# Kernel tuning notes

Measured on AMD Instinct MI355X. Metric: run time of the kernel, lower is better.

## Reference

```python
import jax, jax.numpy as jnp
import numpy as np

B, S, D, H = 4, 2048, 1024, 16
DK = D // H


def setup_inputs() -> dict:
    key = jax.random.key(0)
    kx, kq, kk, kv, ko = jax.random.split(key, 5)
    scale = D ** -0.5
    return {
        "x": jax.random.normal(kx, (B, S, D), dtype=jnp.float32),
        "W_q": jax.random.normal(kq, (D, D), dtype=jnp.float32) * scale,
        "W_k": jax.random.normal(kk, (D, D), dtype=jnp.float32) * scale,
        "W_v": jax.random.normal(kv, (D, D), dtype=jnp.float32) * scale,
        "W_o": jax.random.normal(ko, (D, D), dtype=jnp.float32) * scale,
    }


def reference(x, W_q, W_k, W_v, W_o):
    b, s, d = x.shape
    # projections: x @ W.T  (weights stored [out, in])
    def proj(W):
        return (x @ W.T).reshape(b, s, H, DK).transpose(0, 2, 1, 3)  # [b,h,s,dk]
    Q, K, V = proj(W_q), proj(W_k), proj(W_v)
    scores = jnp.einsum('bhqd,bhkd->bhqk', Q, K) * (DK ** -0.5)
    causal = jnp.tril(jnp.ones((s, s), dtype=bool))
    scores = jnp.where(causal, scores, -jnp.inf)
    attn = jax.nn.softmax(scores, axis=-1)
    out = jnp.einsum('bhqk,bhkd->bhqd', attn, V)  # [b,h,s,dk]
    out = out.transpose(0, 2, 1, 3).reshape(b, s, d)
    return out @ W_o.T
```

## Files before the change

kernel.cpp:

```cpp
#include <hip/hip_runtime.h>
#include <stdint.h>

#define B_ 4
#define S_ 2048
#define D_ 1024
#define H_ 16
#define DK_ 64
#define M_ (B_*S_)

typedef __attribute__((ext_vector_type(8))) short bhalf8;
typedef __attribute__((ext_vector_type(4))) short bhalf4;
typedef __attribute__((ext_vector_type(4))) float floatx4;
typedef unsigned short bfu;
typedef unsigned int u32;

__device__ __forceinline__ bfu f2bf(float f) {
  union { float f; u32 u; } v; v.f = f;
  u32 r = v.u + 0x7FFFu + ((v.u >> 16) & 1u);
  return (bfu)(r >> 16);
}

__device__ __forceinline__ u32 cvtpk(float a, float b) {
  u32 r;
  asm("v_cvt_pk_bf16_f32 %0, %1, %2" : "=v"(r) : "v"(a), "v"(b));
  return r;
}

__device__ __forceinline__ void gll16(const bfu* g, bfu* l) {
  __builtin_amdgcn_global_load_lds((__attribute__((address_space(1))) void*)g,
                                   (__attribute__((address_space(3))) void*)l,
                                   16, 0, 0);
}

__global__ void cvt_f32_bf16(const float* __restrict__ src, bfu* __restrict__ dst, int n) {
  int i = (blockIdx.x * blockDim.x + threadIdx.x) * 4;
  if (i >= n) return;
  float4 v = *(const float4*)(src + i);
  ushort4 o;
  o.x = f2bf(v.x); o.y = f2bf(v.y); o.z = f2bf(v.z); o.w = f2bf(v.w);
  *(ushort4*)(dst + i) = o;
}

__device__ __forceinline__ void gemm_core_gll(const bfu* __restrict__ A,
                                              const bfu* __restrict__ Bw,
                                              bfu* aT, bfu* bT,
                                              int m0, int bn0,
                                              floatx4 (&acc)[4][4])
{
  const int tid  = threadIdx.x;
  const int lane = tid & 63;
  const int g    = lane >> 4;
  const int i16  = lane & 15;
  const int w    = tid >> 6;
  const int wm   = w >> 1, wn = w & 1;

  const int lrow = lane >> 3;
  const int scol = ((lane & 7) ^ lrow) << 3;
  const bfu* As = A  + (size_t)(m0  + w * 32 + lrow) * D_ + scol;
  const bfu* Bs = Bw + (size_t)(bn0 + w * 32 + lrow) * D_ + scol;

  for (int k0 = 0; k0 < D_; k0 += 64) {
#pragma unroll
    for (int j = 0; j < 4; ++j) {
      gll16(As + (size_t)j * 8 * D_ + k0, aT + (w * 4 + j) * 512);
      gll16(Bs + (size_t)j * 8 * D_ + k0, bT + (w * 4 + j) * 512);
    }
    __syncthreads();
    const char* aTc = (const char*)aT;
    const char* bTc = (const char*)bT;
#pragma unroll
    for (int kb = 0; kb < 2; ++kb) {
      bhalf8 af[4], bf[4];
#pragma unroll
      for (int f = 0; f < 4; ++f) {
        int arow = wm * 64 + f * 16 + i16;
        af[f] = *(const bhalf8*)(aTc + arow * 128 + ((kb * 64 + g * 16) ^ ((arow & 7) << 4)));
        int brow = wn * 64 + f * 16 + i16;
        bf[f] = *(const bhalf8*)(bTc + brow * 128 + ((kb * 64 + g * 16) ^ ((brow & 7) << 4)));
      }
#pragma unroll
      for (int fm = 0; fm < 4; ++fm)
#pragma unroll
        for (int fn = 0; fn < 4; ++fn)
          acc[fm][fn] = __builtin_amdgcn_mfma_f32_16x16x32_bf16(af[fm], bf[fn], acc[fm][fn], 0, 0, 0);
    }
    __syncthreads();
  }
}

__global__ __launch_bounds__(256) void qkv_gemm(const bfu* __restrict__ xb,
                                                const bfu* __restrict__ wqkv,
                                                bfu* __restrict__ Qd,
                                                bfu* __restrict__ Kd,
                                                bfu* __restrict__ Vtd)
{
  __shared__ bfu aT[8192], bT[8192];
  const int bid = blockIdx.x;
  const int wi   = bid >> 3;
  const int xblk = wi >> 3;
  const int y    = ((bid & 7) << 3) | (wi & 7);
  const int m0   = y * 128;
  const int z    = xblk >> 3;
  const int n0   = (xblk & 7) * 128;
  const int bn0  = xblk * 128;

  floatx4 acc[4][4] = {};
  gemm_core_gll(xb, wqkv, aT, bT, m0, bn0, acc);

  bfu* dst = (z == 0) ? Qd : (z == 1) ? Kd : Vtd;
  const int lane = threadIdx.x & 63;
  const int g = lane >> 4, i16 = lane & 15;
  const int w = threadIdx.x >> 6, wm = w >> 1, wn = w & 1;
#pragma unroll
  for (int fm = 0; fm < 4; ++fm) {
#pragma unroll
    for (int fn = 0; fn < 4; ++fn) {
      int col = n0 + wn * 64 + fn * 16 + i16;
      int h = col >> 6, dk = col & 63;
#pragma unroll
      for (int r = 0; r < 4; ++r) {
        int mrow = m0 + wm * 64 + fm * 16 + g * 4 + r;
        int b = mrow >> 11, s = mrow & (S_ - 1);
        size_t idx = (z == 2)
            ? ((size_t)((b * H_ + h) * DK_ + dk)) * S_ + s
            : ((size_t)((b * H_ + h) * S_ + s)) * DK_ + dk;
        dst[idx] = f2bf(acc[fm][fn][r]);
      }
    }
  }
}

__global__ __launch_bounds__(256) void out_gemm(const bfu* __restrict__ Ab,
                                                const bfu* __restrict__ wob,
                                                float* __restrict__ out)
{
  __shared__ bfu aT[8192], bT[8192];
  const int bid = blockIdx.x;
  const int wi   = bid >> 3;
  const int xblk = wi >> 3;
  const int y    = ((bid & 7) << 3) | (wi & 7);
  const int m0   = y * 128;
  const int n0   = xblk * 128;

  floatx4 acc[4][4] = {};
  gemm_core_gll(Ab, wob, aT, bT, m0, n0, acc);

  const int lane = threadIdx.x & 63;
  const int g = lane >> 4, i16 = lane & 15;
  const int w = threadIdx.x >> 6, wm = w >> 1, wn = w & 1;
#pragma unroll
  for (int fm = 0; fm < 4; ++fm)
#pragma unroll
    for (int fn = 0; fn < 4; ++fn) {
      int col = n0 + wn * 64 + fn * 16 + i16;
#pragma unroll
      for (int r = 0; r < 4; ++r) {
        int mrow = m0 + wm * 64 + fm * 16 + g * 4 + r;
        out[(size_t)mrow * D_ + col] = acc[fm][fn][r];
      }
    }
}

template<int BUF>
__device__ __forceinline__ void attn_tile(const char* smem, int t, int ntw, int qr,
                                          int koff0, int koff1, const int (&voff)[4],
                                          bhalf8 qa0, bhalf8 qa1, int g, int i16,
                                          floatx4 (&ot)[4], float& mC2, float& lp)
{
  const float C2 = 0.125f * 1.44269504f;
  floatx4 sa[4] = {};
#pragma unroll
  for (int cb = 0; cb < 4; ++cb) {
    bhalf8 kf0 = *(const bhalf8*)(smem + BUF + cb * 2048 + koff0);
    bhalf8 kf1 = *(const bhalf8*)(smem + BUF + cb * 2048 + koff1);
    sa[cb] = __builtin_amdgcn_mfma_f32_16x16x32_bf16(kf0, qa0, sa[cb], 0, 0, 0);
    sa[cb] = __builtin_amdgcn_mfma_f32_16x16x32_bf16(kf1, qa1, sa[cb], 0, 0, 0);
  }
  if (t == ntw - 1) {
    const int kv0 = t * 64;
#pragma unroll
    for (int cb = 0; cb < 4; ++cb)
#pragma unroll
      for (int r = 0; r < 4; ++r)
        if (kv0 + cb * 16 + g * 4 + r > qr + i16) sa[cb][r] = -3.0e38f;
  }
  float pm = sa[0][0];
#pragma unroll
  for (int cb = 0; cb < 4; ++cb)
#pragma unroll
    for (int r = 0; r < 4; ++r)
      pm = fmaxf(pm, sa[cb][r]);
  pm = fmaxf(pm, __shfl_xor(pm, 16));
  pm = fmaxf(pm, __shfl_xor(pm, 32));
  const float pmC2 = pm * C2;
  if (!__all(pmC2 - mC2 <= 8.0f)) {
    const float nmax = fmaxf(mC2, pmC2);
    const float al = exp2f(mC2 - nmax);
    mC2 = nmax;
    lp *= al;
#pragma unroll
    for (int da = 0; da < 4; ++da)
#pragma unroll
      for (int r = 0; r < 4; ++r)
        ot[da][r] *= al;
  }
  const float nm = -mC2;
  u32 pk[8];
  float ps = 0.f;
#pragma unroll
  for (int cb = 0; cb < 4; ++cb) {
    float p0 = exp2f(__builtin_fmaf(sa[cb][0], C2, nm));
    float p1 = exp2f(__builtin_fmaf(sa[cb][1], C2, nm));
    float p2 = exp2f(__builtin_fmaf(sa[cb][2], C2, nm));
    float p3 = exp2f(__builtin_fmaf(sa[cb][3], C2, nm));
    ps += (p0 + p1) + (p2 + p3);
    pk[cb * 2]     = cvtpk(p0, p1);
    pk[cb * 2 + 1] = cvtpk(p2, p3);
  }
  lp += ps;
#pragma unroll
  for (int da = 0; da < 4; ++da) {
#pragma unroll
    for (int cb = 0; cb < 4; ++cb) {
      bhalf4 vf = *(const bhalf4*)(smem + BUF + voff[cb] + da * 2048);
      union { u32 u[2]; bhalf4 h; } pu;
      pu.u[0] = pk[cb * 2]; pu.u[1] = pk[cb * 2 + 1];
      ot[da] = __builtin_amdgcn_mfma_f32_16x16x16bf16_1k(vf, pu.h, ot[da], 0, 0, 0);
    }
  }
}

__global__ __launch_bounds__(512, 4) void attn_kernel(const bfu* __restrict__ Q,
                                                      const bfu* __restrict__ Kc,
                                                      const bfu* __restrict__ Vt,
                                                      bfu* __restrict__ Oc)
{
  __shared__ char smem[2 * 16384];
  const int tid = threadIdx.x;
  const int lane = tid & 63;
  const int w = tid >> 6;
  const int g = lane >> 4, i16 = lane & 15;
  const int sw = (i16 & 7) << 4;
  const int bh = blockIdx.x;
  const int y  = blockIdx.y;
  const int spine = 2 * y + 2;
  const int ntw = 2 * y + 1 + (w >> 2);
  const int qr = y * 128 + w * 16;

  const bfu* Qb = Q  + (size_t)bh * S_ * DK_;
  const bfu* Kb = Kc + (size_t)bh * S_ * DK_;
  const bfu* Vb = Vt + (size_t)bh * DK_ * S_;
  const int b = bh >> 4, h = bh & 15;

  const int srow = tid >> 3;
  const int scolb = (tid & 7) * 16;
  const bfu* kgp = Kb + srow * DK_ + (scolb >> 1);
  const bfu* vgp = Vb + (size_t)srow * S_ + (scolb >> 1);
  const int sswz = scolb ^ ((srow & 7) << 4);
  char* kld = smem + srow * 128 + sswz;
  char* vld = smem + 8192 + srow * 128 + sswz;

  const int koff0 = i16 * 128 + ((g * 16) ^ sw);
  const int koff1 = i16 * 128 + (((64 + g * 16)) ^ sw);
  int voff[4];
#pragma unroll
  for (int cb = 0; cb < 4; ++cb)
    voff[cb] = 8192 + i16 * 128 + ((cb * 32 + g * 8) ^ sw);

  bhalf8 qa0 = *(const bhalf8*)(Qb + (size_t)(qr + i16) * DK_ + g * 8);
  bhalf8 qa1 = *(const bhalf8*)(Qb + (size_t)(qr + i16) * DK_ + 32 + g * 8);

  floatx4 ot[4] = {};
  float mC2 = -1.0e30f;
  float lp  = 0.f;

  bhalf8 kst = *(const bhalf8*)kgp;
  bhalf8 vst = *(const bhalf8*)vgp;
  *(bhalf8*)kld = kst;
  *(bhalf8*)vld = vst;
  __syncthreads();

  const int half = spine >> 1;
  for (int i = 0; ; ++i) {
    const int t0 = 2 * i, t1 = 2 * i + 1;
    const bool more = (i + 1 < half);
    kst = *(const bhalf8*)(kgp + (size_t)t1 * 4096);
    vst = *(const bhalf8*)(vgp + t1 * 64);
    if (t0 < ntw)
      attn_tile<0>(smem, t0, ntw, qr, koff0, koff1, voff, qa0, qa1, g, i16, ot, mC2, lp);
    *(bhalf8*)(kld + 16384) = kst;
    *(bhalf8*)(vld + 16384) = vst;
    __syncthreads();
    if (more) {
      kst = *(const bhalf8*)(kgp + (size_t)(t0 + 2) * 4096);
      vst = *(const bhalf8*)(vgp + (t0 + 2) * 64);
    }
    if (t1 < ntw)
      attn_tile<16384>(smem, t1, ntw, qr, koff0, koff1, voff, qa0, qa1, g, i16, ot, mC2, lp);
    if (!more) break;
    *(bhalf8*)kld = kst;
    *(bhalf8*)vld = vst;
    __syncthreads();
  }

  float lt = lp;
  lt += __shfl_xor(lt, 16);
  lt += __shfl_xor(lt, 32);
  const float rl = 1.0f / lt;
  const size_t rowbase = (size_t)(b * S_ + qr + i16) * D_ + h * 64;
#pragma unroll
  for (int da = 0; da < 4; ++da) {
    union { u32 u[2]; uint2 v; } ov;
    ov.u[0] = cvtpk(ot[da][0] * rl, ot[da][1] * rl);
    ov.u[1] = cvtpk(ot[da][2] * rl, ot[da][3] * rl);
    *(uint2*)(Oc + rowbase + da * 16 + g * 4) = ov.v;
  }
}

extern "C" void kernel_launch(void* const* d_in, const int* in_sizes, int n_in,
                              void* d_out, int out_size, void* d_ws, size_t ws_size,
                              hipStream_t stream)
{
  const float* x  = (const float*)d_in[0];
  const float* wq = (const float*)d_in[1];
  const float* wk = (const float*)d_in[2];
  const float* wv = (const float*)d_in[3];
  const float* wo = (const float*)d_in[4];

  bfu* xb  = (bfu*)d_ws;
  bfu* wqb = xb  + (size_t)M_ * D_;
  bfu* wkb = wqb + (size_t)D_ * D_;
  bfu* wvb = wkb + (size_t)D_ * D_;
  bfu* wob = wvb + (size_t)D_ * D_;
  bfu* Qd  = wob + (size_t)D_ * D_;
  bfu* Kd  = Qd  + (size_t)M_ * D_;
  bfu* Vtd = Kd  + (size_t)M_ * D_;
  bfu* Ad  = Vtd + (size_t)M_ * D_;

  const int thr = 256;
  cvt_f32_bf16<<<(M_ * D_ / 4 + thr - 1) / thr, thr, 0, stream>>>(x, xb, M_ * D_);
  cvt_f32_bf16<<<(D_ * D_ / 4 + thr - 1) / thr, thr, 0, stream>>>(wq, wqb, D_ * D_);
  cvt_f32_bf16<<<(D_ * D_ / 4 + thr - 1) / thr, thr, 0, stream>>>(wk, wkb, D_ * D_);
  cvt_f32_bf16<<<(D_ * D_ / 4 + thr - 1) / thr, thr, 0, stream>>>(wv, wvb, D_ * D_);
  cvt_f32_bf16<<<(D_ * D_ / 4 + thr - 1) / thr, thr, 0, stream>>>(wo, wob, D_ * D_);

  qkv_gemm<<<1536, 256, 0, stream>>>(xb, wqb, Qd, Kd, Vtd);
  attn_kernel<<<dim3(B_ * H_, S_ / 128), 512, 0, stream>>>(Qd, Kd, Vtd, Ad);
  out_gemm<<<512, 256, 0, stream>>>(Ad, wob, (float*)d_out);
}
```

Before: 194.8 us.

## Pair causal query tiles per block, merge conversion kernels, re-swizzle V LDS

The attention grid is halved so each block processes query tile y and its mirror 15-y, balancing causal work across blocks and removing the tail imbalance. The five separate f32-to-bf16 conversion launches are fused into one kernel that indexes into a contiguous workspace. V's shared-memory layout adds an extra swizzle bit, with stores split into two 8-byte halves to reduce bank conflicts. The changes cost fewer blocks in flight and a serialised second pass per block.

```diff
diff --git a/kernel.cpp b/kernel.cpp
--- a/kernel.cpp
+++ b/kernel.cpp
@@ -32,13 +32,24 @@
                                    16, 0, 0);
 }
 
-__global__ void cvt_f32_bf16(const float* __restrict__ src, bfu* __restrict__ dst, int n) {
-  int i = (blockIdx.x * blockDim.x + threadIdx.x) * 4;
-  if (i >= n) return;
-  float4 v = *(const float4*)(src + i);
+__global__ void cvt_all(const float* __restrict__ x,  const float* __restrict__ wq,
+                        const float* __restrict__ wk, const float* __restrict__ wv,
+                        const float* __restrict__ wo, bfu* __restrict__ dst) {
+  const size_t u = ((size_t)blockIdx.x * blockDim.x + threadIdx.x) * 4;
+  const size_t XN = (size_t)M_ * D_;
+  const float* src;
+  if (u < XN) {
+    src = x + u;
+  } else {
+    const size_t v = u - XN;
+    const int wsel = (int)(v >> 20);
+    const size_t off = v & ((size_t)(1u << 20) - 1);
+    src = ((wsel == 0) ? wq : (wsel == 1) ? wk : (wsel == 2) ? wv : wo) + off;
+  }
+  float4 vv = *(const float4*)src;
   ushort4 o;
-  o.x = f2bf(v.x); o.y = f2bf(v.y); o.z = f2bf(v.z); o.w = f2bf(v.w);
-  *(ushort4*)(dst + i) = o;
+  o.x = f2bf(vv.x); o.y = f2bf(vv.y); o.z = f2bf(vv.z); o.w = f2bf(vv.w);
+  *(ushort4*)(dst + u) = o;
 }
 
 __device__ __forceinline__ void gemm_core_gll(const bfu* __restrict__ A,
@@ -242,10 +253,7 @@
   const int g = lane >> 4, i16 = lane & 15;
   const int sw = (i16 & 7) << 4;
   const int bh = blockIdx.x;
-  const int y  = blockIdx.y;
-  const int spine = 2 * y + 2;
-  const int ntw = 2 * y + 1 + (w >> 2);
-  const int qr = y * 128 + w * 16;
+  const int y0 = blockIdx.y;
 
   const bfu* Qb = Q  + (size_t)bh * S_ * DK_;
   const bfu* Kb = Kc + (size_t)bh * S_ * DK_;
@@ -256,64 +264,78 @@
   const int scolb = (tid & 7) * 16;
   const bfu* kgp = Kb + srow * DK_ + (scolb >> 1);
   const bfu* vgp = Vb + (size_t)srow * S_ + (scolb >> 1);
-  const int sswz = scolb ^ ((srow & 7) << 4);
-  char* kld = smem + srow * 128 + sswz;
-  char* vld = smem + 8192 + srow * 128 + sswz;
+  char* kld = smem + srow * 128 + (scolb ^ ((srow & 7) << 4));
+  const int vsw = ((srow & 7) << 4) | (srow & 8);
+  char* vld0 = smem + 8192 + srow * 128 + ((scolb    ) ^ vsw);
+  char* vld1 = smem + 8192 + srow * 128 + ((scolb + 8) ^ vsw);
 
   const int koff0 = i16 * 128 + ((g * 16) ^ sw);
-  const int koff1 = i16 * 128 + (((64 + g * 16)) ^ sw);
+  const int koff1 = i16 * 128 + ((64 + g * 16) ^ sw);
+  const int vswr = sw | (i16 & 8);
   int voff[4];
 #pragma unroll
   for (int cb = 0; cb < 4; ++cb)
-    voff[cb] = 8192 + i16 * 128 + ((cb * 32 + g * 8) ^ sw);
-
-  bhalf8 qa0 = *(const bhalf8*)(Qb + (size_t)(qr + i16) * DK_ + g * 8);
-  bhalf8 qa1 = *(const bhalf8*)(Qb + (size_t)(qr + i16) * DK_ + 32 + g * 8);
-
-  floatx4 ot[4] = {};
-  float mC2 = -1.0e30f;
-  float lp  = 0.f;
-
-  bhalf8 kst = *(const bhalf8*)kgp;
-  bhalf8 vst = *(const bhalf8*)vgp;
-  *(bhalf8*)kld = kst;
-  *(bhalf8*)vld = vst;
-  __syncthreads();
-
-  const int half = spine >> 1;
-  for (int i = 0; ; ++i) {
-    const int t0 = 2 * i, t1 = 2 * i + 1;
-    const bool more = (i + 1 < half);
-    kst = *(const bhalf8*)(kgp + (size_t)t1 * 4096);
-    vst = *(const bhalf8*)(vgp + t1 * 64);
-    if (t0 < ntw)
-      attn_tile<0>(smem, t0, ntw, qr, koff0, koff1, voff, qa0, qa1, g, i16, ot, mC2, lp);
-    *(bhalf8*)(kld + 16384) = kst;
-    *(bhalf8*)(vld + 16384) = vst;
+    voff[cb] = 8192 + i16 * 128 + ((cb * 32 + g * 8) ^ vswr);
+
+  for (int pass = 0; pass < 2; ++pass) {
+    const int y = pass ? (15 - y0) : y0;
+    const int ntw = 2 * y + 1 + (w >> 2);
+    const int qr = y * 128 + w * 16;
+    const int spine = 2 * y + 2;
+
+    bhalf8 qa0 = *(const bhalf8*)(Qb + (size_t)(qr + i16) * DK_ + g * 8);
+    bhalf8 qa1 = *(const bhalf8*)(Qb + (size_t)(qr + i16) * DK_ + 32 + g * 8);
+
+    floatx4 ot[4] = {};
+    float mC2 = -1.0e30f;
+    float lp  = 0.f;
+
+    union { bhalf8 h8; bhalf4 h4[2]; } vu;
+    bhalf8 kst = *(const bhalf8*)kgp;
+    bhalf8 vst = *(const bhalf8*)vgp;
+    *(bhalf8*)kld = kst;
+    vu.h8 = vst;
+    *(bhalf4*)vld0 = vu.h4[0]; *(bhalf4*)vld1 = vu.h4[1];
     __syncthreads();
-    if (more) {
-      kst = *(const bhalf8*)(kgp + (size_t)(t0 + 2) * 4096);
-      vst = *(const bhalf8*)(vgp + (t0 + 2) * 64);
-    }
-    if (t1 < ntw)
-      attn_tile<16384>(smem, t1, ntw, qr, koff0, koff1, voff, qa0, qa1, g, i16, ot, mC2, lp);
-    if (!more) break;
-    *(bhalf8*)kld = kst;
-    *(bhalf8*)vld = vst;
+
+    const int half = spine >> 1;
+    for (int i = 0; ; ++i) {
+      const int t0 = 2 * i, t1 = 2 * i + 1;
+      const bool more = (i + 1 < half);
+      kst = *(const bhalf8*)(kgp + (size_t)t1 * 4096);
+      vst = *(const bhalf8*)(vgp + t1 * 64);
+      if (t0 < ntw)
+        attn_tile<0>(smem, t0, ntw, qr, koff0, koff1, voff, qa0, qa1, g, i16, ot, mC2, lp);
+      *(bhalf8*)(kld + 16384) = kst;
+      vu.h8 = vst;
+      *(bhalf4*)(vld0 + 16384) = vu.h4[0]; *(bhalf4*)(vld1 + 16384) = vu.h4[1];
+      __syncthreads();
+      if (more) {
+        kst = *(const bhalf8*)(kgp + (size_t)(t0 + 2) * 4096);
+        vst = *(const bhalf8*)(vgp + (t0 + 2) * 64);
+      }
+      if (t1 < ntw)
+        attn_tile<16384>(smem, t1, ntw, qr, koff0, koff1, voff, qa0, qa1, g, i16, ot, mC2, lp);
+      if (!more) break;
+      *(bhalf8*)kld = kst;
+      vu.h8 = vst;
+      *(bhalf4*)vld0 = vu.h4[0]; *(bhalf4*)vld1 = vu.h4[1];
+      __syncthreads();
+    }
     __syncthreads();
-  }
-
-  float lt = lp;
-  lt += __shfl_xor(lt, 16);
-  lt += __shfl_xor(lt, 32);
-  const float rl = 1.0f / lt;
-  const size_t rowbase = (size_t)(b * S_ + qr + i16) * D_ + h * 64;
-#pragma unroll
-  for (int da = 0; da < 4; ++da) {
-    union { u32 u[2]; uint2 v; } ov;
-    ov.u[0] = cvtpk(ot[da][0] * rl, ot[da][1] * rl);
-    ov.u[1] = cvtpk(ot[da][2] * rl, ot[da][3] * rl);
-    *(uint2*)(Oc + rowbase + da * 16 + g * 4) = ov.v;
+
+    float lt = lp;
+    lt += __shfl_xor(lt, 16);
+    lt += __shfl_xor(lt, 32);
+    const float rl = 1.0f / lt;
+    const size_t rowbase = (size_t)(b * S_ + qr + i16) * D_ + h * 64;
+#pragma unroll
+    for (int da = 0; da < 4; ++da) {
+      union { u32 u[2]; uint2 v; } ov;
+      ov.u[0] = cvtpk(ot[da][0] * rl, ot[da][1] * rl);
+      ov.u[1] = cvtpk(ot[da][2] * rl, ot[da][3] * rl);
+      *(uint2*)(Oc + rowbase + da * 16 + g * 4) = ov.v;
+    }
   }
 }
 
@@ -329,22 +351,16 @@
 
   bfu* xb  = (bfu*)d_ws;
   bfu* wqb = xb  + (size_t)M_ * D_;
-  bfu* wkb = wqb + (size_t)D_ * D_;
-  bfu* wvb = wkb + (size_t)D_ * D_;
-  bfu* wob = wvb + (size_t)D_ * D_;
+  bfu* wob = wqb + (size_t)3 * D_ * D_;
   bfu* Qd  = wob + (size_t)D_ * D_;
   bfu* Kd  = Qd  + (size_t)M_ * D_;
   bfu* Vtd = Kd  + (size_t)M_ * D_;
   bfu* Ad  = Vtd + (size_t)M_ * D_;
 
-  const int thr = 256;
-  cvt_f32_bf16<<<(M_ * D_ / 4 + thr - 1) / thr, thr, 0, stream>>>(x, xb, M_ * D_);
-  cvt_f32_bf16<<<(D_ * D_ / 4 + thr - 1) / thr, thr, 0, stream>>>(wq, wqb, D_ * D_);
-  cvt_f32_bf16<<<(D_ * D_ / 4 + thr - 1) / thr, thr, 0, stream>>>(wk, wkb, D_ * D_);
-  cvt_f32_bf16<<<(D_ * D_ / 4 + thr - 1) / thr, thr, 0, stream>>>(wv, wvb, D_ * D_);
-  cvt_f32_bf16<<<(D_ * D_ / 4 + thr - 1) / thr, thr, 0, stream>>>(wo, wob, D_ * D_);
+  const size_t total = (size_t)M_ * D_ + 4 * (size_t)D_ * D_;
+  cvt_all<<<(int)(total / 4 / 256), 256, 0, stream>>>(x, wq, wk, wv, wo, xb);
 
   qkv_gemm<<<1536, 256, 0, stream>>>(xb, wqb, Qd, Kd, Vtd);
-  attn_kernel<<<dim3(B_ * H_, S_ / 128), 512, 0, stream>>>(Qd, Kd, Vtd, Ad);
+  attn_kernel<<<dim3(B_ * H_, 8), 512, 0, stream>>>(Qd, Kd, Vtd, Ad);
   out_gemm<<<512, 256, 0, stream>>>(Ad, wob, (float*)d_out);
 }
```

New measurement: 177.4 us. -8.9%, faster.
